# Kernel tuning notes

Measured on AMD Instinct MI355X. Metric: run time of the kernel, lower is better.

## Reference

```python
import jax, jax.numpy as jnp
import numpy as np

K = 3       # kernel_size
STRIDE = 1
PAD = 1


def conv3d(x, w, b):
    # standard Conv3d NCDHW, used to predict per-tap offsets
    y = jax.lax.conv_general_dilated(
        x, w, window_strides=(STRIDE,) * 3, padding=[(PAD, PAD)] * 3,
        dimension_numbers=("NCDHW", "OIDHW", "NCDHW"))
    return y + b[None, :, None, None, None]


def trilinear_sample(xn, pd, ph, pw):
    # xn: (C,D,H,W); pd/ph/pw: (T,Do,Ho,Wo) float voxel coords.
    # Trilinear interpolation with zeros padding (grid_sample semantics).
    C, D, H, W = xn.shape
    d0 = jnp.floor(pd); h0 = jnp.floor(ph); w0 = jnp.floor(pw)
    fd = pd - d0; fh = ph - h0; fw = pw - w0
    d0 = d0.astype(jnp.int32); h0 = h0.astype(jnp.int32); w0 = w0.astype(jnp.int32)
    out = jnp.zeros((C,) + pd.shape, xn.dtype)
    for dd in (0, 1):
        wd = fd if dd else 1.0 - fd
        di = d0 + dd
        for hh in (0, 1):
            wh = fh if hh else 1.0 - fh
            hi = h0 + hh
            for ww in (0, 1):
                wc = fw if ww else 1.0 - fw
                wi = w0 + ww
                valid = (di >= 0) & (di < D) & (hi >= 0) & (hi < H) & (wi >= 0) & (wi < W)
                wgt = jnp.where(valid, wd * wh * wc, 0.0)
                g = xn[:, jnp.clip(di, 0, D - 1), jnp.clip(hi, 0, H - 1), jnp.clip(wi, 0, W - 1)]
                out = out + wgt[None] * g
    return out  # (C,T,Do,Ho,Wo)


def deform_conv3d(x, offset, weight):
    # x: (N,C,D,H,W); offset: (N,3*K^3,Do,Ho,Wo); weight: (O,C,K,K,K)
    N, C, D, H, W = x.shape
    Do = (D + 2 * PAD - K) // STRIDE + 1
    Ho = (H + 2 * PAD - K) // STRIDE + 1
    Wo = (W + 2 * PAD - K) // STRIDE + 1
    T = K ** 3
    kd, kh, kw = jnp.meshgrid(jnp.arange(K), jnp.arange(K), jnp.arange(K), indexing="ij")
    kd = kd.reshape(T, 1, 1, 1).astype(x.dtype)
    kh = kh.reshape(T, 1, 1, 1).astype(x.dtype)
    kw = kw.reshape(T, 1, 1, 1).astype(x.dtype)
    base_d = kd - PAD + (jnp.arange(Do, dtype=x.dtype) * STRIDE).reshape(1, Do, 1, 1)
    base_h = kh - PAD + (jnp.arange(Ho, dtype=x.dtype) * STRIDE).reshape(1, 1, Ho, 1)
    base_w = kw - PAD + (jnp.arange(Wo, dtype=x.dtype) * STRIDE).reshape(1, 1, 1, Wo)
    off = offset.reshape(N, 3, T, Do, Ho, Wo)  # matches offset.view(N,3,K,K,K,...) tap ordering
    pd = base_d[None] + off[:, 0]
    ph = base_h[None] + off[:, 1]
    pw = base_w[None] + off[:, 2]
    sampled = jax.vmap(trilinear_sample)(x, pd, ph, pw)  # (N,C,T,Do,Ho,Wo)
    O = weight.shape[0]
    w2 = weight.reshape(O, C, T)
    return jnp.einsum("nctdhw,oct->nodhw", sampled, w2)


def setup_inputs() -> dict:
    key = jax.random.key(0)
    k1, k2, k3 = jax.random.split(key, 3)
    N, C, O, S = 2, 16, 32, 48
    x = jax.random.normal(k1, (N, C, S, S, S), jnp.float32)
    fan_in = C * K ** 3
    weight = jax.random.normal(k2, (O, C, K, K, K), jnp.float32) * (1.0 / np.sqrt(fan_in))
    # offset conv params; small scale so sampled positions stay near the base grid
    offset_w = jax.random.normal(k3, (3 * K ** 3, C, K, K, K), jnp.float32) * 0.02
    offset_b = jnp.zeros((3 * K ** 3,), jnp.float32)
    return {"x": x, "weight": weight, "offset_w": offset_w, "offset_b": offset_b}


def reference(x, weight, offset_w, offset_b):
    offset = conv3d(x, offset_w, offset_b)
    return deform_conv3d(x, offset, weight)
```

## Files before the change

kernel.cpp:

```cpp
#include <hip/hip_runtime.h>
#include <hip/hip_bf16.h>

#define SDIM 48
#define SP   110592
#define C_IN 16
#define O_OUT 32
#define T27  27
#define G81  81

typedef __attribute__((ext_vector_type(8))) short bf16x8;
typedef __attribute__((ext_vector_type(4))) float f32x4;
typedef __attribute__((ext_vector_type(2))) float f32x2;

__device__ __forceinline__ float bf2f(unsigned short u) {
    unsigned int x = ((unsigned int)u) << 16;
    return __builtin_bit_cast(float, x);
}
__device__ __forceinline__ unsigned short f2bf(float f) {
    unsigned int x = __builtin_bit_cast(unsigned int, f);
    x += 0x7fffu + ((x >> 16) & 1u);
    return (unsigned short)(x >> 16);
}

__global__ __launch_bounds__(256)
void prep_xT(const float* __restrict__ x, unsigned short* __restrict__ xT) {
    __shared__ float l[256 * 17];
    const int tid = threadIdx.x;
    const int b   = blockIdx.x;
    const int n   = b / 432;
    const int sp0 = (b - n * 432) * 256;
    #pragma unroll
    for (int c = 0; c < 16; ++c)
        l[tid * 17 + c] = x[((size_t)(n * 16 + c)) * SP + sp0 + tid];
    __syncthreads();
    unsigned int u[8];
    #pragma unroll
    for (int q = 0; q < 8; ++q) {
        unsigned short a = f2bf(l[tid * 17 + 2 * q]);
        unsigned short bb = f2bf(l[tid * 17 + 2 * q + 1]);
        u[q] = (unsigned int)a | ((unsigned int)bb << 16);
    }
    uint4* dst = (uint4*)(xT + ((size_t)(n * SP + sp0 + tid)) * 16);
    dst[0] = make_uint4(u[0], u[1], u[2], u[3]);
    dst[1] = make_uint4(u[4], u[5], u[6], u[7]);
}

__global__ __launch_bounds__(256)
void prep_bfrag(const float* __restrict__ ow, unsigned short* __restrict__ Bf) {
    int idx = blockIdx.x * 256 + threadIdx.x;
    int r    = idx & 7;
    int lane = (idx >> 3) & 63;
    int snt  = idx >> 9;
    int s = snt / 6, nt = snt - s * 6;
    int kk  = ((lane >> 4) << 3) + r;
    int g   = nt * 16 + (lane & 15);
    int tap = 2 * s + (kk >> 4);
    int c   = kk & 15;
    float v = 0.f;
    if (tap < 27 && g < 81) v = ow[((size_t)(g * 16 + c)) * 27 + tap];
    Bf[idx] = f2bf(v);
}

__global__ __launch_bounds__(256)
void prep_wfrag(const float* __restrict__ w, unsigned short* __restrict__ Wf) {
    int idx = blockIdx.x * 256 + threadIdx.x;
    int r    = idx & 7;
    int lane = (idx >> 3) & 63;
    int snt  = idx >> 9;
    int s = snt >> 1, nt = snt & 1;
    int kk  = ((lane >> 4) << 3) + r;
    int o   = nt * 16 + (lane & 15);
    int tap = 2 * s + (kk >> 4);
    int c   = kk & 15;
    float v = 0.f;
    if (tap < 27) v = w[((size_t)(o * 16 + c)) * 27 + tap];
    Wf[idx] = f2bf(v);
}

__global__ __launch_bounds__(256)
void offs_conv_mfma(const unsigned short* __restrict__ xT,
                    const unsigned short* __restrict__ Bf,
                    const float* __restrict__ ob,
                    unsigned short* __restrict__ offs) {
    __shared__ unsigned short Alds[256 * 8];
    const int tid  = threadIdx.x;
    const int lane = tid & 63;
    const int wid  = tid >> 6;
    const int j    = wid;
    const int m    = tid & 63;
    const int gm   = blockIdx.x * 64 + m;
    const int n    = (gm >= SP) ? 1 : 0;
    const int sp   = gm - n * SP;
    const int z    = sp / 2304;
    const int rem  = sp - z * 2304;
    const int y    = rem / 48;
    const int xx   = rem - y * 48;
    const int tapoff = j >> 1;
    const int half   = j & 1;

    auto stage_load = [&](int s) -> uint4 {
        int tap = 2 * s + tapoff;
        int kd = tap / 9;
        int t2 = tap - kd * 9;
        int kh = t2 / 3;
        int kw = t2 - kh * 3;
        int di = z + kd - 1, hi = y + kh - 1, wi = xx + kw - 1;
        bool ok = (tap < 27) && ((unsigned)di < 48u) && ((unsigned)hi < 48u) &&
                  ((unsigned)wi < 48u);
        uint4 v = make_uint4(0u, 0u, 0u, 0u);
        if (ok) {
            size_t off = ((size_t)(n * SP + (di * 2304 + hi * 48 + wi))) * 16 + half * 8;
            v = *(const uint4*)(xT + off);
        }
        return v;
    };

    f32x4 acc[6];
    #pragma unroll
    for (int t = 0; t < 6; ++t) acc[t] = (f32x4){0.f, 0.f, 0.f, 0.f};

    uint4 v = stage_load(0);
    for (int s = 0; s < 14; ++s) {
        __syncthreads();
        *(uint4*)&Alds[tid * 8] = v;
        __syncthreads();
        if (s < 13) v = stage_load(s + 1);
        bf16x8 a = *(const bf16x8*)&Alds[(((lane >> 4) * 64) + (wid * 16) + (lane & 15)) * 8];
        const bf16x8* bp = (const bf16x8*)Bf + (size_t)(s * 6) * 64 + lane;
        #pragma unroll
        for (int nt = 0; nt < 6; ++nt) {
            bf16x8 b = bp[nt * 64];
            acc[nt] = __builtin_amdgcn_mfma_f32_16x16x32_bf16(a, b, acc[nt], 0, 0, 0);
        }
    }

    const int mrow = wid * 16 + ((lane >> 4) << 2);
    const int gmr  = blockIdx.x * 64 + mrow;
    const int n2   = (gmr >= SP) ? 1 : 0;
    const int spr  = gmr - n2 * SP;
    #pragma unroll
    for (int nt = 0; nt < 6; ++nt) {
        int g = nt * 16 + (lane & 15);
        if (g < 81) {
            float bia = ob[g];
            unsigned short h0 = f2bf(acc[nt][0] + bia);
            unsigned short h1 = f2bf(acc[nt][1] + bia);
            unsigned short h2 = f2bf(acc[nt][2] + bia);
            unsigned short h3 = f2bf(acc[nt][3] + bia);
            uint2 pv;
            pv.x = (unsigned int)h0 | ((unsigned int)h1 << 16);
            pv.y = (unsigned int)h2 | ((unsigned int)h3 << 16);
            *(uint2*)(offs + ((size_t)(n2 * 81 + g)) * SP + spr) = pv;
        }
    }
}

__global__ __launch_bounds__(256, 4)
void deform_mfma(const unsigned short* __restrict__ xT,
                 const unsigned short* __restrict__ Wf,
                 const unsigned short* __restrict__ offs,
                 float* __restrict__ out) {
    __shared__ unsigned short Alds[4 * 64 * 24];
    __shared__ float olds[32 * 65];
    const int tid  = threadIdx.x;
    const int lane = tid & 63;
    const int wid  = tid >> 6;
    const int m    = lane;
    const int n    = (blockIdx.x >= 1728) ? 1 : 0;
    const int sp0  = blockIdx.x * 64 - n * SP;
    const int sp   = sp0 + m;
    const int z    = sp / 2304;
    const int rm   = sp - z * 2304;
    const int y    = rm / 48;
    const int xx   = rm - y * 48;

    const unsigned short* offn = offs + (size_t)n * G81 * SP + sp;
    const uint4* xq4 = (const uint4*)(xT + (size_t)n * SP * 16);

    struct Stg { uint4 a, b; };

    auto stage = [&](int rr) -> Stg {
        Stg res;
        res.a = make_uint4(0u, 0u, 0u, 0u);
        res.b = make_uint4(0u, 0u, 0u, 0u);
        const int tap = 4 * rr + wid;
        if (tap >= 27) return res;
        const int kd = tap / 9;
        const int t2 = tap - kd * 9;
        const int kh = t2 / 3;
        const int kw = t2 - kh * 3;
        float pd = (float)(z + kd - 1)  + bf2f(offn[(size_t)tap * SP]);
        float ph = (float)(y + kh - 1)  + bf2f(offn[(size_t)(27 + tap) * SP]);
        float pw = (float)(xx + kw - 1) + bf2f(offn[(size_t)(54 + tap) * SP]);
        float df = floorf(pd), hf = floorf(ph), wf = floorf(pw);
        float fd = pd - df, fh = ph - hf, fw = pw - wf;
        int d0 = (int)df, h0 = (int)hf, w0 = (int)wf;
        float wd0 = ((unsigned)d0       < 48u) ? (1.f - fd) : 0.f;
        float wd1 = ((unsigned)(d0 + 1) < 48u) ? fd : 0.f;
        float wh0 = ((unsigned)h0       < 48u) ? (1.f - fh) : 0.f;
        float wh1 = ((unsigned)(h0 + 1) < 48u) ? fh : 0.f;
        float ww0 = ((unsigned)w0       < 48u) ? (1.f - fw) : 0.f;
        float ww1 = ((unsigned)(w0 + 1) < 48u) ? fw : 0.f;
        int dc0 = min(max(d0,     0), 47) * 2304;
        int dc1 = min(max(d0 + 1, 0), 47) * 2304;
        int hc0 = min(max(h0,     0), 47) * 48;
        int hc1 = min(max(h0 + 1, 0), 47) * 48;
        int wc0 = min(max(w0,     0), 47);
        int wc1 = min(max(w0 + 1, 0), 47);

        float wdh[4] = {wd0 * wh0, wd0 * wh1, wd1 * wh0, wd1 * wh1};
        int   rdh[4] = {dc0 + hc0, dc0 + hc1, dc1 + hc0, dc1 + hc1};

        f32x2 s2v[8];
        #pragma unroll
        for (int q = 0; q < 8; ++q) s2v[q] = (f32x2){0.f, 0.f};

        #pragma unroll
        for (int g2 = 0; g2 < 2; ++g2) {
            uint4 cv[8];
            float cwt[4];
            #pragma unroll
            for (int pidx = 0; pidx < 2; ++pidx) {
                int jj = g2 * 2 + pidx;
                int i0 = rdh[jj] + wc0;
                int i1 = rdh[jj] + wc1;
                cv[pidx * 4 + 0] = xq4[(size_t)i0 * 2];
                cv[pidx * 4 + 1] = xq4[(size_t)i0 * 2 + 1];
                cv[pidx * 4 + 2] = xq4[(size_t)i1 * 2];
                cv[pidx * 4 + 3] = xq4[(size_t)i1 * 2 + 1];
                cwt[pidx * 2 + 0] = wdh[jj] * ww0;
                cwt[pidx * 2 + 1] = wdh[jj] * ww1;
            }
            #pragma unroll
            for (int pidx = 0; pidx < 2; ++pidx) {
                #pragma unroll
                for (int wsel = 0; wsel < 2; ++wsel) {
                    f32x2 w2;
                    w2.x = cwt[pidx * 2 + wsel];
                    w2.y = w2.x;
                    const uint4& lo4 = cv[pidx * 4 + wsel * 2];
                    const uint4& hi4 = cv[pidx * 4 + wsel * 2 + 1];
                    unsigned int wd_[8] = {lo4.x, lo4.y, lo4.z, lo4.w,
                                           hi4.x, hi4.y, hi4.z, hi4.w};
                    #pragma unroll
                    for (int q = 0; q < 8; ++q) {
                        f32x2 xv;
                        xv.x = __builtin_bit_cast(float, wd_[q] << 16);
                        xv.y = __builtin_bit_cast(float, wd_[q] & 0xffff0000u);
                        s2v[q] = __builtin_elementwise_fma(xv, w2, s2v[q]);
                    }
                }
            }
        }
        unsigned int o_[8];
        #pragma unroll
        for (int q = 0; q < 8; ++q) {
            unsigned int r_;
            asm("v_cvt_pk_bf16_f32 %0, %1, %2" : "=v"(r_) : "v"(s2v[q].x), "v"(s2v[q].y));
            o_[q] = r_;
        }
        res.a = make_uint4(o_[0], o_[1], o_[2], o_[3]);
        res.b = make_uint4(o_[4], o_[5], o_[6], o_[7]);
        return res;
    };

    f32x4 acc0 = (f32x4){0.f, 0.f, 0.f, 0.f};
    f32x4 acc1 = (f32x4){0.f, 0.f, 0.f, 0.f};

    const int q_   = lane >> 4;
    const int tl   = q_ >> 1;
    const int chh  = q_ & 1;
    const int rowm = wid * 16 + (lane & 15);

    Stg v = stage(0);
    for (int rr = 0; rr < 7; ++rr) {
        __syncthreads();
        unsigned short* wp_ = &Alds[(wid * 64 + m) * 24];
        *(uint4*)wp_ = v.a;
        *(uint4*)(wp_ + 8) = v.b;
        __syncthreads();
        if (rr < 6) v = stage(rr + 1);
        bf16x8 a0 = *(const bf16x8*)&Alds[((tl * 64) + rowm) * 24 + chh * 8];
        bf16x8 a1 = *(const bf16x8*)&Alds[(((2 + tl) * 64) + rowm) * 24 + chh * 8];
        const bf16x8* bp0 = (const bf16x8*)Wf + (size_t)((2 * rr + 0) * 2) * 64 + lane;
        const bf16x8* bp1 = (const bf16x8*)Wf + (size_t)((2 * rr + 1) * 2) * 64 + lane;
        acc0 = __builtin_amdgcn_mfma_f32_16x16x32_bf16(a0, bp0[0],  acc0, 0, 0, 0);
        acc1 = __builtin_amdgcn_mfma_f32_16x16x32_bf16(a0, bp0[64], acc1, 0, 0, 0);
        acc0 = __builtin_amdgcn_mfma_f32_16x16x32_bf16(a1, bp1[0],  acc0, 0, 0, 0);
        acc1 = __builtin_amdgcn_mfma_f32_16x16x32_bf16(a1, bp1[64], acc1, 0, 0, 0);
    }

    __syncthreads();
    const int mr = wid * 16 + ((lane >> 4) << 2);
    {
        int o = lane & 15;
        #pragma unroll
        for (int r = 0; r < 4; ++r) olds[o * 65 + mr + r] = acc0[r];
        #pragma unroll
        for (int r = 0; r < 4; ++r) olds[(16 + o) * 65 + mr + r] = acc1[r];
    }
    __syncthreads();
    const int o  = tid >> 3;
    const int m8 = (tid & 7) * 8;
    float* op = out + ((size_t)(n * O_OUT + o)) * SP + sp0 + m8;
    float4 a0s = make_float4(olds[o * 65 + m8],     olds[o * 65 + m8 + 1],
                             olds[o * 65 + m8 + 2], olds[o * 65 + m8 + 3]);
    float4 a1s = make_float4(olds[o * 65 + m8 + 4], olds[o * 65 + m8 + 5],
                             olds[o * 65 + m8 + 6], olds[o * 65 + m8 + 7]);
    *(float4*)op       = a0s;
    *(float4*)(op + 4) = a1s;
}

extern "C" void kernel_launch(void* const* d_in, const int* in_sizes, int n_in,
                              void* d_out, int out_size, void* d_ws, size_t ws_size,
                              hipStream_t stream) {
    (void)in_sizes; (void)n_in; (void)out_size; (void)ws_size;
    const float* x      = (const float*)d_in[0];
    const float* weight = (const float*)d_in[1];
    const float* ow     = (const float*)d_in[2];
    const float* ob     = (const float*)d_in[3];
    float* out = (float*)d_out;

    unsigned short* offs_b = (unsigned short*)d_ws;
    unsigned short* xT     = offs_b + (size_t)2 * 81 * SP;
    unsigned short* Bf     = xT + (size_t)2 * SP * 16;
    unsigned short* Wf     = Bf + 43008;

    prep_xT<<<864, 256, 0, stream>>>(x, xT);
    prep_bfrag<<<168, 256, 0, stream>>>(ow, Bf);
    prep_wfrag<<<56, 256, 0, stream>>>(weight, Wf);
    offs_conv_mfma<<<3456, 256, 0, stream>>>(xT, Bf, ob, offs_b);
    deform_mfma<<<3456, 256, 0, stream>>>(xT, Wf, offs_b, out);
}
```

Measured before the change: 171.8 us.

## Restructure deform kernel to 16-voxel blocks with one thread per tap

Each block of the deformable-conv kernel now covers 16 output voxels with 448 threads, one thread per (voxel, tap), instead of 64 voxels looping over taps in 7 staged rounds. All 27 taps are sampled in parallel, and each wave performs a split-K MFMA over two K-slices. The seven partial results are then reduced through shared memory. This removes the serial per-round stage/sync pipeline and raises parallelism, but it adds a cross-wave reduction, shorter 64-byte output rows, and four times as many blocks.

Measured after the change: 170.0 us. Within noise of the previous version (-1.1%).

```diff
diff --git a/kernel.cpp b/kernel.cpp
--- a/kernel.cpp
+++ b/kernel.cpp
@@ -155,20 +155,23 @@
     }
 }
 
-__global__ __launch_bounds__(256, 4)
-void deform_mfma(const unsigned short* __restrict__ xT,
-                 const unsigned short* __restrict__ Wf,
-                 const unsigned short* __restrict__ offs,
-                 float* __restrict__ out) {
-    __shared__ unsigned short Alds[4 * 64 * 24];
-    __shared__ float olds[32 * 65];
+__global__ __launch_bounds__(448, 7)
+void deform_fused(const unsigned short* __restrict__ xT,
+                  const unsigned short* __restrict__ Wf,
+                  const unsigned short* __restrict__ offs,
+                  float* __restrict__ out) {
+    __shared__ __align__(16) unsigned char smem[17920];
+    unsigned short* S  = (unsigned short*)smem;
+    float*          Cp = (float*)smem;
+
     const int tid  = threadIdx.x;
     const int lane = tid & 63;
-    const int wid  = tid >> 6;
-    const int m    = lane;
-    const int n    = (blockIdx.x >= 1728) ? 1 : 0;
-    const int sp0  = blockIdx.x * 64 - n * SP;
-    const int sp   = sp0 + m;
+    const int wv   = tid >> 6;
+    const int p    = tid & 15;
+    const int t    = tid >> 4;
+    const int n    = (blockIdx.x >= 6912) ? 1 : 0;
+    const int sp0  = blockIdx.x * 16 - n * SP;
+    const int sp   = sp0 + p;
     const int z    = sp / 2304;
     const int rm   = sp - z * 2304;
     const int y    = rm / 48;
@@ -177,21 +180,16 @@
     const unsigned short* offn = offs + (size_t)n * G81 * SP + sp;
     const uint4* xq4 = (const uint4*)(xT + (size_t)n * SP * 16);
 
-    struct Stg { uint4 a, b; };
-
-    auto stage = [&](int rr) -> Stg {
-        Stg res;
-        res.a = make_uint4(0u, 0u, 0u, 0u);
-        res.b = make_uint4(0u, 0u, 0u, 0u);
-        const int tap = 4 * rr + wid;
-        if (tap >= 27) return res;
-        const int kd = tap / 9;
-        const int t2 = tap - kd * 9;
+    uint4 ra = make_uint4(0u, 0u, 0u, 0u);
+    uint4 rb = make_uint4(0u, 0u, 0u, 0u);
+    if (t < 27) {
+        const int kd = t / 9;
+        const int t2 = t - kd * 9;
         const int kh = t2 / 3;
         const int kw = t2 - kh * 3;
-        float pd = (float)(z + kd - 1)  + bf2f(offn[(size_t)tap * SP]);
-        float ph = (float)(y + kh - 1)  + bf2f(offn[(size_t)(27 + tap) * SP]);
-        float pw = (float)(xx + kw - 1) + bf2f(offn[(size_t)(54 + tap) * SP]);
+        float pd = (float)(z + kd - 1)  + bf2f(offn[(size_t)t * SP]);
+        float ph = (float)(y + kh - 1)  + bf2f(offn[(size_t)(27 + t) * SP]);
+        float pw = (float)(xx + kw - 1) + bf2f(offn[(size_t)(54 + t) * SP]);
         float df = floorf(pd), hf = floorf(ph), wf = floorf(pw);
         float fd = pd - df, fh = ph - hf, fw = pw - wf;
         int d0 = (int)df, h0 = (int)hf, w0 = (int)wf;
@@ -259,56 +257,54 @@
             asm("v_cvt_pk_bf16_f32 %0, %1, %2" : "=v"(r_) : "v"(s2v[q].x), "v"(s2v[q].y));
             o_[q] = r_;
         }
-        res.a = make_uint4(o_[0], o_[1], o_[2], o_[3]);
-        res.b = make_uint4(o_[4], o_[5], o_[6], o_[7]);
-        return res;
-    };
+        ra = make_uint4(o_[0], o_[1], o_[2], o_[3]);
+        rb = make_uint4(o_[4], o_[5], o_[6], o_[7]);
+    }
+    {
+        unsigned short* wp_ = S + p * 488 + t * 16;
+        *(uint4*)wp_       = ra;
+        *(uint4*)(wp_ + 8) = rb;
+    }
+    __syncthreads();
 
     f32x4 acc0 = (f32x4){0.f, 0.f, 0.f, 0.f};
     f32x4 acc1 = (f32x4){0.f, 0.f, 0.f, 0.f};
-
-    const int q_   = lane >> 4;
-    const int tl   = q_ >> 1;
-    const int chh  = q_ & 1;
-    const int rowm = wid * 16 + (lane & 15);
-
-    Stg v = stage(0);
-    for (int rr = 0; rr < 7; ++rr) {
-        __syncthreads();
-        unsigned short* wp_ = &Alds[(wid * 64 + m) * 24];
-        *(uint4*)wp_ = v.a;
-        *(uint4*)(wp_ + 8) = v.b;
-        __syncthreads();
-        if (rr < 6) v = stage(rr + 1);
-        bf16x8 a0 = *(const bf16x8*)&Alds[((tl * 64) + rowm) * 24 + chh * 8];
-        bf16x8 a1 = *(const bf16x8*)&Alds[(((2 + tl) * 64) + rowm) * 24 + chh * 8];
-        const bf16x8* bp0 = (const bf16x8*)Wf + (size_t)((2 * rr + 0) * 2) * 64 + lane;
-        const bf16x8* bp1 = (const bf16x8*)Wf + (size_t)((2 * rr + 1) * 2) * 64 + lane;
+    {
+        const int q   = lane >> 4;
+        const int pr  = lane & 15;
+        const int ks0 = 2 * wv;
+        bf16x8 a0 = *(const bf16x8*)(S + pr * 488 + ks0 * 32 + q * 8);
+        bf16x8 a1 = *(const bf16x8*)(S + pr * 488 + (ks0 + 1) * 32 + q * 8);
+        const bf16x8* bp0 = (const bf16x8*)Wf + (size_t)((ks0 + 0) * 2) * 64 + lane;
+        const bf16x8* bp1 = (const bf16x8*)Wf + (size_t)((ks0 + 1) * 2) * 64 + lane;
         acc0 = __builtin_amdgcn_mfma_f32_16x16x32_bf16(a0, bp0[0],  acc0, 0, 0, 0);
         acc1 = __builtin_amdgcn_mfma_f32_16x16x32_bf16(a0, bp0[64], acc1, 0, 0, 0);
         acc0 = __builtin_amdgcn_mfma_f32_16x16x32_bf16(a1, bp1[0],  acc0, 0, 0, 0);
         acc1 = __builtin_amdgcn_mfma_f32_16x16x32_bf16(a1, bp1[64], acc1, 0, 0, 0);
     }
-
     __syncthreads();
-    const int mr = wid * 16 + ((lane >> 4) << 2);
+
     {
-        int o = lane & 15;
-        #pragma unroll
-        for (int r = 0; r < 4; ++r) olds[o * 65 + mr + r] = acc0[r];
-        #pragma unroll
-        for (int r = 0; r < 4; ++r) olds[(16 + o) * 65 + mr + r] = acc1[r];
+        const int o16 = lane & 15;
+        const int m0  = (lane >> 4) << 2;
+        *(f32x4*)&Cp[(wv * 32 + o16)      * 20 + m0] = acc0;
+        *(f32x4*)&Cp[(wv * 32 + 16 + o16) * 20 + m0] = acc1;
     }
     __syncthreads();
-    const int o  = tid >> 3;
-    const int m8 = (tid & 7) * 8;
-    float* op = out + ((size_t)(n * O_OUT + o)) * SP + sp0 + m8;
-    float4 a0s = make_float4(olds[o * 65 + m8],     olds[o * 65 + m8 + 1],
-                             olds[o * 65 + m8 + 2], olds[o * 65 + m8 + 3]);
-    float4 a1s = make_float4(olds[o * 65 + m8 + 4], olds[o * 65 + m8 + 5],
-                             olds[o * 65 + m8 + 6], olds[o * 65 + m8 + 7]);
-    *(float4*)op       = a0s;
-    *(float4*)(op + 4) = a1s;
+
+    #pragma unroll
+    for (int rep = 0; rep < 2; ++rep) {
+        int idx = tid + rep * 448;
+        if (rep == 0 || tid < 64) {
+            int o = idx >> 4;
+            int m = idx & 15;
+            float r0 = 0.f;
+            #pragma unroll
+            for (int w2 = 0; w2 < 7; ++w2)
+                r0 += Cp[(w2 * 32 + o) * 20 + m];
+            out[((size_t)(n * O_OUT + o)) * SP + sp0 + m] = r0;
+        }
+    }
 }
 
 extern "C" void kernel_launch(void* const* d_in, const int* in_sizes, int n_in,
@@ -330,5 +326,5 @@
     prep_bfrag<<<168, 256, 0, stream>>>(ow, Bf);
     prep_wfrag<<<56, 256, 0, stream>>>(weight, Wf);
     offs_conv_mfma<<<3456, 256, 0, stream>>>(xT, Bf, ob, offs_b);
-    deform_mfma<<<3456, 256, 0, stream>>>(xT, Wf, offs_b, out);
-}
+    deform_fused<<<13824, 448, 0, stream>>>(xT, Wf, offs_b, out);
+}
```
